# Kernel optimization log

Hardware: AMD Instinct MI355X
Metric: run time of the kernel (lower is better)

## Reference

```python
import jax, jax.numpy as jnp
import numpy as np
from jax import lax

DILATIONS = [2 ** i for i in range(9)] * 5  # 45 layers
RD, SD, QD, KF = 32, 512, 256, 33  # residual, skip, quantization channels, causal kernel
PAD = int(np.sum(DILATIONS)) + KF // 2  # 2571
L_IN = 165142  # finallen = L_IN - 2*PAD = 160000


def conv1d(x, w, b, d=1):
    # x: [N, Cin, L], w: [Cout, Cin, K] -> [N, Cout, L - d*(K-1)] (VALID)
    y = lax.conv_general_dilated(x, w, window_strides=(1,), padding='VALID',
                                 rhs_dilation=(d,),
                                 dimension_numbers=('NCH', 'OIH', 'NCH'))
    return y + b[None, :, None]


def setup_inputs() -> dict:
    key = jax.random.key(0)
    ks = jax.random.split(key, 16)
    f = lambda k, s: jax.random.normal(k, s, dtype=jnp.float32) * 0.1
    return {
        'x': jax.random.normal(ks[0], (1, 1, L_IN), dtype=jnp.float32),
        'w_causal': f(ks[1], (RD, 1, KF)), 'b_causal': f(ks[2], (RD,)),
        'w_tanh': f(ks[3], (45, RD, RD, 3)), 'b_tanh': f(ks[4], (45, RD)),
        'w_sig': f(ks[5], (45, RD, RD, 3)), 'b_sig': f(ks[6], (45, RD)),
        'w_skip': f(ks[7], (45, SD, RD, 1)), 'b_skip': f(ks[8], (45, SD)),
        'w_dense': f(ks[9], (45, RD, RD, 1)), 'b_dense': f(ks[10], (45, RD)),
        'w_post1': f(ks[11], (SD, SD, 1)), 'b_post1': f(ks[12], (SD,)),
        'w_post2': f(ks[13], (QD, SD, 1)), 'b_post2': f(ks[14], (QD,)),
    }


def reference(x, w_causal, b_causal, w_tanh, b_tanh, w_sig, b_sig,
              w_skip, b_skip, w_dense, b_dense,
              w_post1, b_post1, w_post2, b_post2):
    finallen = x.shape[-1] - 2 * PAD  # static
    x = conv1d(x, w_causal, b_causal)  # [1, RD, L-32]
    skip = jnp.zeros((1, SD, finallen), dtype=jnp.float32)
    for i, d in enumerate(DILATIONS):  # fixed 45-layer stack
        xin = x[:, :, d:-d]  # residual path, matches VALID dilated conv output length
        x1 = jnp.tanh(conv1d(x, w_tanh[i], b_tanh[i], d))
        x2 = jax.nn.sigmoid(conv1d(x, w_sig[i], b_sig[i], d))
        x = x1 * x2
        cut = (x.shape[-1] - finallen) // 2  # static
        s = conv1d(x, w_skip[i], b_skip[i])  # [1, SD, cur_len]
        skip = skip + s[:, :, cut:cut + finallen]
        x = conv1d(x, w_dense[i], b_dense[i]) + xin
    h = jax.nn.relu(conv1d(jax.nn.relu(skip), w_post1, b_post1))
    return conv1d(h, w_post2, b_post2)  # [1, QD, finallen]
```

## Files before the change

### kernel.cpp

```cpp
#include <hip/hip_runtime.h>
#include <hip/hip_bf16.h>
#include <cstdio>

typedef unsigned short ushort_t;
typedef __bf16 bf16x8 __attribute__((ext_vector_type(8)));
typedef float f32x4 __attribute__((ext_vector_type(4)));

#define FL   160000
#define L0   165110
#define NL   45
#define CH   80000

__device__ __forceinline__ float tanh_fast(float x) {
    float ax = fabsf(x);
    float e  = __expf(-2.f * ax);
    float r  = (1.f - e) / (1.f + e);
    return copysignf(r, x);
}
__device__ __forceinline__ float sigmoid_fast(float x) {
    return 1.f / (1.f + __expf(-x));
}

#define GLOAD_LDS16(gp, lp) \
    __builtin_amdgcn_global_load_lds( \
        (const __attribute__((address_space(1))) void*)(gp), \
        (__attribute__((address_space(3))) void*)(lp), 16, 0, 0)

__global__ __launch_bounds__(256) void causal_kernel(
    const float* __restrict__ x, const float* __restrict__ wc,
    const float* __restrict__ bc, float* __restrict__ y)
{
    __shared__ float ws_[33 * 32];
    __shared__ float bs_[32];
    const int tid = threadIdx.x;
    for (int idx = tid; idx < 33 * 32; idx += 256) {
        int k = idx >> 5, oc = idx & 31;
        ws_[idx] = wc[oc * 33 + k];
    }
    if (tid < 32) bs_[tid] = bc[tid];
    __syncthreads();
    const int t = blockIdx.x * 256 + tid;
    if (t >= L0) return;
    float acc[32];
#pragma unroll
    for (int oc = 0; oc < 32; ++oc) acc[oc] = bs_[oc];
    for (int k = 0; k < 33; ++k) {
        float xv = x[t + k];
        const float* wp = &ws_[k * 32];
#pragma unroll
        for (int oc = 0; oc < 32; ++oc) acc[oc] += wp[oc] * xv;
    }
    float* yr = y + (size_t)t * 32;
#pragma unroll
    for (int oc = 0; oc < 32; oc += 4)
        *(float4*)(yr + oc) = make_float4(acc[oc], acc[oc+1], acc[oc+2], acc[oc+3]);
}

__global__ __launch_bounds__(256) void prepack_frag(
    const float* __restrict__ wt, const float* __restrict__ wsg,
    const float* __restrict__ wd,
    __bf16* __restrict__ fragConv, __bf16* __restrict__ fragDense)
{
    const int idx = blockIdx.x * 256 + threadIdx.x;
    if (idx < NL * 12 * 64) {
        const int lane = idx & 63;
        const int rem  = idx >> 6;
        const int slot = rem % 12, l = rem / 12;
        const int j = slot >> 2, i = slot & 3;
        const int m = (i & 1) * 16 + (lane & 15);
        const int quad = lane >> 4;
        const float* wsrc = (i < 2) ? wt : wsg;
        __bf16 v[8];
#pragma unroll
        for (int jj = 0; jj < 8; ++jj) {
            int ic = quad * 8 + jj;
            v[jj] = (__bf16)wsrc[((size_t)(l * 32 + m) * 32 + ic) * 3 + j];
        }
        *(uint4*)(fragConv + (size_t)idx * 8) = *(const uint4*)v;
    }
    if (idx < NL * 2 * 64) {
        const int lane = idx & 63;
        const int rem  = idx >> 6;
        const int i = rem & 1, l = rem >> 1;
        const int m = i * 16 + (lane & 15);
        const int quad = lane >> 4;
        __bf16 v[8];
#pragma unroll
        for (int jj = 0; jj < 8; ++jj)
            v[jj] = (__bf16)wd[(size_t)(l * 32 + m) * 32 + quad * 8 + jj];
        *(uint4*)(fragDense + (size_t)idx * 8) = *(const uint4*)v;
    }
}

__global__ __launch_bounds__(256) void layer_mfma(
    const float* __restrict__ xin,
    float* __restrict__ xout,
    __bf16* __restrict__ xslot,
    const __bf16* __restrict__ fragConv,
    const __bf16* __restrict__ fragDense,
    const float* __restrict__ bt, const float* __restrict__ bs,
    const float* __restrict__ bd,
    int d, int Lout, int S)
{
    __shared__ __bf16 gbuf[4][32][40];
    const int tid  = threadIdx.x;
    const int wave = tid >> 6, lane = tid & 63;
    const int fm = lane & 15, quad = lane >> 4;
    const int t0 = blockIdx.x * 128 + wave * 32;

    bf16x8 Ac[3][4], Ad[2];
#pragma unroll
    for (int j = 0; j < 3; ++j)
#pragma unroll
        for (int i = 0; i < 4; ++i)
            Ac[j][i] = *(const bf16x8*)(fragConv + ((j * 4 + i) * 64 + lane) * 8);
#pragma unroll
    for (int i = 0; i < 2; ++i)
        Ad[i] = *(const bf16x8*)(fragDense + (i * 64 + lane) * 8);

    f32x4 acc[4][2];
#pragma unroll
    for (int i = 0; i < 4; ++i) {
        const float* bb = (i < 2) ? (bt + i * 16) : (bs + (i - 2) * 16);
        float4 b4 = *(const float4*)(bb + quad * 4);
        f32x4 bi; bi[0] = b4.x; bi[1] = b4.y; bi[2] = b4.z; bi[3] = b4.w;
        acc[i][0] = bi; acc[i][1] = bi;
    }

#pragma unroll
    for (int j2 = 0; j2 < 2; ++j2) {
        int tl = t0 + j2 * 16 + fm;
        if (tl > Lout - 1) tl = Lout - 1;
#pragma unroll
        for (int j = 0; j < 3; ++j) {
            const float* xp = xin + (size_t)(tl + j * d) * 32 + quad * 8;
            float4 u0 = *(const float4*)xp;
            float4 u1 = *(const float4*)(xp + 4);
            bf16x8 bf;
            bf[0] = (__bf16)u0.x; bf[1] = (__bf16)u0.y;
            bf[2] = (__bf16)u0.z; bf[3] = (__bf16)u0.w;
            bf[4] = (__bf16)u1.x; bf[5] = (__bf16)u1.y;
            bf[6] = (__bf16)u1.z; bf[7] = (__bf16)u1.w;
#pragma unroll
            for (int i = 0; i < 4; ++i)
                acc[i][j2] = __builtin_amdgcn_mfma_f32_16x16x32_bf16(
                    Ac[j][i], bf, acc[i][j2], 0, 0, 0);
        }
    }

#pragma unroll
    for (int i = 0; i < 2; ++i)
#pragma unroll
        for (int j2 = 0; j2 < 2; ++j2) {
            __bf16 pk[4];
#pragma unroll
            for (int r = 0; r < 4; ++r)
                pk[r] = (__bf16)(tanh_fast(acc[i][j2][r]) *
                                 sigmoid_fast(acc[i + 2][j2][r]));
            *(uint2*)&gbuf[wave][j2 * 16 + fm][i * 16 + quad * 4] =
                *(const uint2*)pk;
        }

    {
        const int rr = lane >> 1, hh = lane & 1;
        const int t = t0 + rr, tw = t - S;
        if (t < Lout && (unsigned)tw < FL) {
            const char* gp = (const char*)&gbuf[wave][rr][0] + hh * 32;
            uint4 v0 = *(const uint4*)gp;
            uint4 v1 = *(const uint4*)(gp + 16);
            uint4* dst = (uint4*)(xslot + (size_t)tw * 32 + hh * 16);
            dst[0] = v0; dst[1] = v1;
        }
    }

    f32x4 dacc[2][2];
#pragma unroll
    for (int i = 0; i < 2; ++i) {
        float4 b4 = *(const float4*)(bd + i * 16 + quad * 4);
        f32x4 bi; bi[0] = b4.x; bi[1] = b4.y; bi[2] = b4.z; bi[3] = b4.w;
        dacc[i][0] = bi; dacc[i][1] = bi;
    }
#pragma unroll
    for (int j2 = 0; j2 < 2; ++j2) {
        bf16x8 gb = *(const bf16x8*)&gbuf[wave][j2 * 16 + fm][quad * 8];
#pragma unroll
        for (int i = 0; i < 2; ++i)
            dacc[i][j2] = __builtin_amdgcn_mfma_f32_16x16x32_bf16(
                Ad[i], gb, dacc[i][j2], 0, 0, 0);
    }
#pragma unroll
    for (int i = 0; i < 2; ++i)
#pragma unroll
        for (int j2 = 0; j2 < 2; ++j2) {
            const int t = t0 + j2 * 16 + fm;
            if (t < Lout) {
                const int oc = i * 16 + quad * 4;
                float4 r4 = *(const float4*)(xin + (size_t)(t + d) * 32 + oc);
                float4 o;
                o.x = dacc[i][j2][0] + r4.x;
                o.y = dacc[i][j2][1] + r4.y;
                o.z = dacc[i][j2][2] + r4.z;
                o.w = dacc[i][j2][3] + r4.w;
                *(float4*)(xout + (size_t)t * 32 + oc) = o;
            }
        }
}

template<bool TSTORE>
__global__ __launch_bounds__(512, 2) void gemm256(
    const __bf16* __restrict__ A, const __bf16* __restrict__ Bt,
    void* __restrict__ Cout, int ldc,
    const float* __restrict__ bias, int K, int Ncur, int mTile,
    int ldRow, size_t kStrA, size_t kStrB)
{
    __shared__ __bf16 lds[4 * 16384];
    const int tid  = threadIdx.x;
    const int wave = tid >> 6, lane = tid & 63;
    const int fm = lane & 15, quad = lane >> 4;
    const int wm = wave >> 2, wn = wave & 3;

    const int nwg = gridDim.x;
    const int q8 = nwg >> 3, r8 = nwg & 7;
    const int xcd = blockIdx.x & 7, loc = blockIdx.x >> 3;
    const int sbid = (xcd < r8 ? xcd * (q8 + 1)
                               : r8 * (q8 + 1) + (xcd - r8) * q8) + loc;
    const int m0 = (sbid % mTile) * 256;
    const int n0 = (sbid / mTile) * 256;

    const __bf16* pS[4];
    int dstE[4];
#pragma unroll
    for (int i = 0; i < 4; ++i) {
        const int cidx = (i & 1) * 512 + tid;
        const int r = cidx >> 2, c = cidx & 3;
        const int cs = c ^ ((r >> 1) & 3);
        if (i < 2) {
            pS[i] = A + (size_t)(m0 + r) * ldRow + cs * 8;
        } else {
            int rg = n0 + r; if (rg > Ncur - 1) rg = Ncur - 1;
            pS[i] = Bt + (size_t)rg * ldRow + cs * 8;
        }
        dstE[i] = ((i < 2) ? 0 : 8192) + (i & 1) * 4096 + wave * 512;
    }

    const int swz = ((quad ^ ((fm >> 1) & 3)) << 3);
    const int aoff = (wm * 128 + fm) * 32 + swz;
    const int boff = 8192 + (wn * 64 + fm) * 32 + swz;

    f32x4 acc[8][4] = {};

    auto do_stage = [&](int t) {
        const int pb = (t & 3) * 16384;
        const size_t ka = (size_t)t * kStrA;
        const size_t kb = (size_t)t * kStrB;
        GLOAD_LDS16(pS[0] + ka, lds + pb + dstE[0]);
        GLOAD_LDS16(pS[1] + ka, lds + pb + dstE[1]);
        GLOAD_LDS16(pS[2] + kb, lds + pb + dstE[2]);
        GLOAD_LDS16(pS[3] + kb, lds + pb + dstE[3]);
    };
    auto tile_compute = [&](int t) {
        const int pb = (t & 3) * 16384;
        bf16x8 af[8], bg[4];
#pragma unroll
        for (int i = 0; i < 8; ++i)
            af[i] = *(const bf16x8*)(lds + pb + aoff + i * 512);
#pragma unroll
        for (int j = 0; j < 4; ++j)
            bg[j] = *(const bf16x8*)(lds + pb + boff + j * 512);
        __builtin_amdgcn_s_setprio(1);
#pragma unroll
        for (int i = 0; i < 8; ++i)
#pragma unroll
            for (int j = 0; j < 4; ++j)
                acc[i][j] = __builtin_amdgcn_mfma_f32_16x16x32_bf16(
                    af[i], bg[j], acc[i][j], 0, 0, 0);
        __builtin_amdgcn_s_setprio(0);
    };

    const int NT = K >> 5;
    do_stage(0); do_stage(1); do_stage(2);
    for (int t = 0; t < NT - 3; ++t) {
        asm volatile("s_waitcnt vmcnt(8)" ::: "memory");
        __builtin_amdgcn_s_barrier();
        __builtin_amdgcn_sched_barrier(0);
        do_stage(t + 3);
        tile_compute(t);
    }
    asm volatile("s_waitcnt vmcnt(8)" ::: "memory");
    __builtin_amdgcn_s_barrier();
    __builtin_amdgcn_sched_barrier(0);
    tile_compute(NT - 3);
    asm volatile("s_waitcnt vmcnt(4)" ::: "memory");
    __builtin_amdgcn_s_barrier();
    __builtin_amdgcn_sched_barrier(0);
    tile_compute(NT - 2);
    asm volatile("s_waitcnt vmcnt(0)" ::: "memory");
    __builtin_amdgcn_s_barrier();
    __builtin_amdgcn_sched_barrier(0);
    tile_compute(NT - 1);

    if (TSTORE) {
        __bf16* O = (__bf16*)Cout;
#pragma unroll
        for (int i = 0; i < 8; ++i) {
            const int m = m0 + wm * 128 + i * 16 + quad * 4;
            const float4 bv = *(const float4*)(bias + m);
#pragma unroll
            for (int j = 0; j < 4; ++j) {
                const int n = n0 + wn * 64 + j * 16 + fm;
                if (n < Ncur) {
                    __bf16 pk[4];
                    pk[0] = (__bf16)fmaxf(acc[i][j][0] + bv.x, 0.f);
                    pk[1] = (__bf16)fmaxf(acc[i][j][1] + bv.y, 0.f);
                    pk[2] = (__bf16)fmaxf(acc[i][j][2] + bv.z, 0.f);
                    pk[3] = (__bf16)fmaxf(acc[i][j][3] + bv.w, 0.f);
                    *(uint2*)(O + (size_t)n * ldc + m) = *(const uint2*)pk;
                }
            }
        }
    } else {
        float* O = (float*)Cout;
#pragma unroll
        for (int i = 0; i < 8; ++i) {
            const int m = m0 + wm * 128 + i * 16 + quad * 4;
            const float4 bv = *(const float4*)(bias + m);
#pragma unroll
            for (int j = 0; j < 4; ++j) {
                const int n = n0 + wn * 64 + j * 16 + fm;
                if (n < Ncur) {
                    O[(size_t)(m + 0) * ldc + n] = acc[i][j][0] + bv.x;
                    O[(size_t)(m + 1) * ldc + n] = acc[i][j][1] + bv.y;
                    O[(size_t)(m + 2) * ldc + n] = acc[i][j][2] + bv.z;
                    O[(size_t)(m + 3) * ldc + n] = acc[i][j][3] + bv.w;
                }
            }
        }
    }
}

__global__ __launch_bounds__(256) void repack_kernel(
    const float* __restrict__ wskip, const float* __restrict__ bskip,
    __bf16* __restrict__ wcat, float* __restrict__ bsum)
{
    const int idx = blockIdx.x * 256 + threadIdx.x;
    if (idx < NL * 512 * 32) wcat[idx] = (__bf16)wskip[idx];
    if (idx < 512) {
        float s = 0.f;
        for (int l = 0; l < NL; ++l) s += bskip[l * 512 + idx];
        bsum[idx] = s;
    }
}

__global__ __launch_bounds__(256) void repack_post(
    const float* __restrict__ w1, const float* __restrict__ w2,
    __bf16* __restrict__ wp1, __bf16* __restrict__ wp2)
{
    const int idx = blockIdx.x * 256 + threadIdx.x;
    if (idx < 512 * 512) wp1[idx] = (__bf16)w1[idx];
    if (idx < 256 * 512) wp2[idx] = (__bf16)w2[idx];
}

extern "C" void kernel_launch(void* const* d_in, const int* in_sizes, int n_in,
                              void* d_out, int out_size, void* d_ws, size_t ws_size,
                              hipStream_t stream)
{
    const float* x        = (const float*)d_in[0];
    const float* w_causal = (const float*)d_in[1];
    const float* b_causal = (const float*)d_in[2];
    const float* w_tanh   = (const float*)d_in[3];
    const float* b_tanh   = (const float*)d_in[4];
    const float* w_sig    = (const float*)d_in[5];
    const float* b_sig    = (const float*)d_in[6];
    const float* w_skip   = (const float*)d_in[7];
    const float* b_skip   = (const float*)d_in[8];
    const float* w_dense  = (const float*)d_in[9];
    const float* b_dense  = (const float*)d_in[10];
    const float* w_post1  = (const float*)d_in[11];
    const float* b_post1  = (const float*)d_in[12];
    const float* w_post2  = (const float*)d_in[13];
    const float* b_post2  = (const float*)d_in[14];
    float* out = (float*)d_out;

    char* base = (char*)d_ws;
    __bf16* XcatT2 = (__bf16*)base;
    __bf16* skipTc = (__bf16*)(base + 460800000);
    __bf16* hTc    = (__bf16*)(base + 542720000);
    __bf16* wcat2  = (__bf16*)(base + 624640000);
    __bf16* wp1    = (__bf16*)(base + 626114560);
    __bf16* wp2    = (__bf16*)(base + 626638848);
    float*  bsum   = (float*)(base + 626900992);
    __bf16* fragConv  = (__bf16*)(base + 626903040);
    __bf16* fragDense = (__bf16*)(base + 627456000);
    float*  xb0    = (float*)(base + 460800000);
    float*  xb1    = (float*)(base + 460800000 + 21135360);
    const size_t need = 627548160;
    if (ws_size < need) {
        fprintf(stderr, "kernel_launch: ws_size %zu < needed %zu\n", ws_size, need);
        return;
    }

    repack_kernel<<<2880, 256, 0, stream>>>(w_skip, b_skip, wcat2, bsum);
    repack_post<<<1024, 256, 0, stream>>>(w_post1, w_post2, wp1, wp2);
    prepack_frag<<<(NL * 12 * 64 + 255) / 256, 256, 0, stream>>>(
        w_tanh, w_sig, w_dense, fragConv, fragDense);
    causal_kernel<<<(L0 + 255) / 256, 256, 0, stream>>>(x, w_causal, b_causal, xb0);

    int Lin = L0;
    int S   = 2555;
    float* xc = xb0;
    float* xn = xb1;
    for (int l = 0; l < NL; ++l) {
        const int d = 1 << (l % 9);
        const int Lout = Lin - 2 * d;
        S -= d;
        layer_mfma<<<(Lout + 127) / 128, 256, 0, stream>>>(
            xc, xn, XcatT2 + (size_t)l * FL * 32,
            fragConv + (size_t)l * 12 * 64 * 8,
            fragDense + (size_t)l * 2 * 64 * 8,
            b_tanh + l * 32, b_sig + l * 32, b_dense + l * 32,
            d, Lout, S);
        float* tmp = xc; xc = xn; xn = tmp;
        Lin = Lout;
    }

    const int nTile = (CH + 255) / 256;
    for (int c = 0; c < 2; ++c) {
        const int c0 = c * CH;
        gemm256<true><<<nTile * 2, 512, 0, stream>>>(
            wcat2, XcatT2 + (size_t)c0 * 32, skipTc, 512, bsum,
            1440, CH, 2, 32, (size_t)512 * 32, (size_t)FL * 32);
        gemm256<true><<<nTile * 2, 512, 0, stream>>>(
            wp1, skipTc, hTc, 512, b_post1, 512, CH, 2, 512, 32, 32);
        gemm256<false><<<nTile, 512, 0, stream>>>(
            wp2, hTc, out + c0, FL, b_post2, 512, CH, 1, 512, 32, 32);
    }
}
```

Measured before the change: 1.580 ms.

## Split GEMM tile compute into interleaved halves and swizzle layer blocks across XCDs

The GEMM main loop now splits each K-tile into two halves. Each half loads its A fragments, issues part of the next stage's global-to-LDS loads, then runs its MFMAs, with extra barriers between the halves. The goal is to interleave memory issue with MFMA work and to reduce register pressure by holding only 4 A fragments at a time. Separately, the layer kernel remaps block indices so consecutive time tiles land on the same XCD, which should improve L2 locality. The additional barriers add synchronisation cost.

```diff
diff --git a/kernel.cpp b/kernel.cpp
--- a/kernel.cpp
+++ b/kernel.cpp
@@ -106,7 +106,13 @@
     const int tid  = threadIdx.x;
     const int wave = tid >> 6, lane = tid & 63;
     const int fm = lane & 15, quad = lane >> 4;
-    const int t0 = blockIdx.x * 128 + wave * 32;
+
+    const int nwg = gridDim.x;
+    const int q8 = nwg >> 3, r8 = nwg & 7;
+    const int xcd = blockIdx.x & 7, loc = blockIdx.x >> 3;
+    const int bswz = (xcd < r8 ? xcd * (q8 + 1)
+                               : r8 * (q8 + 1) + (xcd - r8) * q8) + loc;
+    const int t0 = bswz * 128 + wave * 32;
 
     bf16x8 Ac[3][4], Ad[2];
 #pragma unroll
@@ -249,55 +255,76 @@
 
     f32x4 acc[8][4] = {};
 
-    auto do_stage = [&](int t) {
+    auto do_stageA = [&](int t) {
         const int pb = (t & 3) * 16384;
         const size_t ka = (size_t)t * kStrA;
-        const size_t kb = (size_t)t * kStrB;
         GLOAD_LDS16(pS[0] + ka, lds + pb + dstE[0]);
         GLOAD_LDS16(pS[1] + ka, lds + pb + dstE[1]);
+    };
+    auto do_stageB = [&](int t) {
+        const int pb = (t & 3) * 16384;
+        const size_t kb = (size_t)t * kStrB;
         GLOAD_LDS16(pS[2] + kb, lds + pb + dstE[2]);
         GLOAD_LDS16(pS[3] + kb, lds + pb + dstE[3]);
     };
-    auto tile_compute = [&](int t) {
+
+    auto tile_body = [&](int t, bool st, int gate) {
         const int pb = (t & 3) * 16384;
-        bf16x8 af[8], bg[4];
-#pragma unroll
-        for (int i = 0; i < 8; ++i)
+        bf16x8 af[4], bg[4];
+#pragma unroll
+        for (int i = 0; i < 4; ++i)
             af[i] = *(const bf16x8*)(lds + pb + aoff + i * 512);
 #pragma unroll
         for (int j = 0; j < 4; ++j)
             bg[j] = *(const bf16x8*)(lds + pb + boff + j * 512);
+        if (st) do_stageA(t + 3);
+        __builtin_amdgcn_s_barrier();
+        asm volatile("s_waitcnt lgkmcnt(0)" ::: "memory");
+        __builtin_amdgcn_sched_barrier(0);
         __builtin_amdgcn_s_setprio(1);
 #pragma unroll
-        for (int i = 0; i < 8; ++i)
+        for (int i = 0; i < 4; ++i)
 #pragma unroll
             for (int j = 0; j < 4; ++j)
                 acc[i][j] = __builtin_amdgcn_mfma_f32_16x16x32_bf16(
                     af[i], bg[j], acc[i][j], 0, 0, 0);
         __builtin_amdgcn_s_setprio(0);
+        __builtin_amdgcn_s_barrier();
+#pragma unroll
+        for (int i = 0; i < 4; ++i)
+            af[i] = *(const bf16x8*)(lds + pb + aoff + (i + 4) * 512);
+        if (st) do_stageB(t + 3);
+        __builtin_amdgcn_s_barrier();
+        asm volatile("s_waitcnt lgkmcnt(0)" ::: "memory");
+        __builtin_amdgcn_sched_barrier(0);
+        __builtin_amdgcn_s_setprio(1);
+#pragma unroll
+        for (int i = 0; i < 4; ++i)
+#pragma unroll
+            for (int j = 0; j < 4; ++j)
+                acc[i + 4][j] = __builtin_amdgcn_mfma_f32_16x16x32_bf16(
+                    af[i], bg[j], acc[i + 4][j], 0, 0, 0);
+        __builtin_amdgcn_s_setprio(0);
+        if (gate == 8)      asm volatile("s_waitcnt vmcnt(8)" ::: "memory");
+        else if (gate == 4) asm volatile("s_waitcnt vmcnt(4)" ::: "memory");
+        else if (gate == 0) asm volatile("s_waitcnt vmcnt(0)" ::: "memory");
+        if (gate >= 0) {
+            __builtin_amdgcn_s_barrier();
+            __builtin_amdgcn_sched_barrier(0);
+        }
     };
 
     const int NT = K >> 5;
-    do_stage(0); do_stage(1); do_stage(2);
-    for (int t = 0; t < NT - 3; ++t) {
-        asm volatile("s_waitcnt vmcnt(8)" ::: "memory");
-        __builtin_amdgcn_s_barrier();
-        __builtin_amdgcn_sched_barrier(0);
-        do_stage(t + 3);
-        tile_compute(t);
-    }
+    do_stageA(0); do_stageB(0);
+    do_stageA(1); do_stageB(1);
+    do_stageA(2); do_stageB(2);
     asm volatile("s_waitcnt vmcnt(8)" ::: "memory");
     __builtin_amdgcn_s_barrier();
     __builtin_amdgcn_sched_barrier(0);
-    tile_compute(NT - 3);
-    asm volatile("s_waitcnt vmcnt(4)" ::: "memory");
-    __builtin_amdgcn_s_barrier();
-    __builtin_amdgcn_sched_barrier(0);
-    tile_compute(NT - 2);
-    asm volatile("s_waitcnt vmcnt(0)" ::: "memory");
-    __builtin_amdgcn_s_barrier();
-    __builtin_amdgcn_sched_barrier(0);
-    tile_compute(NT - 1);
+    for (int t = 0; t < NT - 3; ++t) tile_body(t, true, 8);
+    tile_body(NT - 3, false, 4);
+    tile_body(NT - 2, false, 0);
+    tile_body(NT - 1, false, -1);
 
     if (TSTORE) {
         __bf16* O = (__bf16*)Cout;
```

Result: no change. 1.576 ms (-0.2%).
